# Optimization experiments

Measured on AMD Instinct MI355X. Metric: run time of the kernel, lower is better.

## Reference

```python
import jax, jax.numpy as jnp
import numpy as np

_K_MASK = float(jnp.finfo(jnp.float32).min)
EPS = 1e-6
B, T, D = 2, 2048, 2048
NH, NKV, HD = 16, 4, 128


def _rope_tables(key):
    # Standard RoPE tables: (B, T, HD) with [freqs, freqs] layout (rotate_half convention)
    inv_freq = 1.0 / (10000.0 ** (np.arange(0, HD, 2, dtype=np.float32) / HD))  # (HD/2,)
    pos = np.arange(T, dtype=np.float32)
    freqs = np.einsum('t,f->tf', pos, inv_freq)              # (T, HD/2)
    emb = np.concatenate([freqs, freqs], axis=-1)            # (T, HD)
    cos = jnp.broadcast_to(jnp.cos(emb)[None], (B, T, HD))
    sin = jnp.broadcast_to(jnp.sin(emb)[None], (B, T, HD))
    return cos, sin


def setup_inputs() -> dict:
    key = jax.random.key(0)
    ks = jax.random.split(key, 6)
    s = 0.02
    cos, sin = _rope_tables(key)
    return {
        'x': jax.random.normal(ks[0], (B, T, D), jnp.float32),
        'cos': cos,
        'sin': sin,
        'wq': jax.random.normal(ks[1], (D, NH * HD * 2), jnp.float32) * s,
        'wk': jax.random.normal(ks[2], (D, NKV * HD), jnp.float32) * s,
        'wv': jax.random.normal(ks[3], (D, NKV * HD), jnp.float32) * s,
        'wo': jax.random.normal(ks[4], (NH * HD, D), jnp.float32) * s,
        'q_norm_w': jnp.ones((HD,), jnp.float32),
        'k_norm_w': jnp.ones((HD,), jnp.float32),
        'segment_ids': jnp.ones((B, T), jnp.int32),
        'position_ids': jnp.broadcast_to(jnp.arange(T, dtype=jnp.int32)[None], (B, T)),
    }


def _rmsnorm(x, w):
    var = jnp.mean(jnp.square(x.astype(jnp.float32)), axis=-1, keepdims=True)
    return (x.astype(jnp.float32) * jax.lax.rsqrt(var + EPS)).astype(x.dtype) * w


def _rotate_half(x):
    x1, x2 = jnp.split(x, 2, axis=-1)
    return jnp.concatenate([-x2, x1], axis=-1)


def _apply_rope(q, k, cos, sin):
    # q: (B, NH, T, HD), k: (B, NKV, T, HD), cos/sin: (B, T, HD)
    c = cos[:, None, :, :]
    s = sin[:, None, :, :]
    q = q * c + _rotate_half(q) * s
    k = k * c + _rotate_half(k) * s
    return q, k


def reference(x, cos, sin, wq, wk, wv, wo, q_norm_w, k_norm_w, segment_ids, position_ids):
    Bx, Tx, _ = x.shape
    n_rep = NH // NKV
    scale = HD ** -0.5

    q_out = (x @ wq).reshape(Bx, Tx, NH, HD * 2)
    query, gate = jnp.split(q_out, 2, axis=-1)         # each (B, T, NH, HD)
    gate = gate.reshape(Bx, Tx, -1)                    # (B, T, NH*HD)
    query = _rmsnorm(query, q_norm_w).transpose(0, 2, 1, 3)   # (B, NH, T, HD)
    key = _rmsnorm((x @ wk).reshape(Bx, Tx, NKV, HD), k_norm_w).transpose(0, 2, 1, 3)
    value = (x @ wv).reshape(Bx, Tx, NKV, HD).transpose(0, 2, 1, 3)

    query, key = _apply_rope(query, key, cos, sin)
    if n_rep > 1:
        key = jnp.repeat(key, n_rep, axis=1)
        value = jnp.repeat(value, n_rep, axis=1)

    attn_logits = jnp.einsum('bhqd,bhkd->bhqk', query, key) * scale
    causal = position_ids[:, :, None] >= position_ids[:, None, :]
    seg = segment_ids[:, :, None] == segment_ids[:, None, :]
    mask = (causal & seg)[:, None, :, :]
    attn_logits = jnp.where(mask, attn_logits, _K_MASK)
    attn_weights = jax.nn.softmax(attn_logits.astype(jnp.float32), axis=-1).astype(attn_logits.dtype)
    attn_out = jnp.einsum('bhqk,bhkd->bhqd', attn_weights, value)
    attn_out = attn_out.transpose(0, 2, 1, 3).reshape(Bx, Tx, -1)  # (B, T, NH*HD)
    attn_out = attn_out * jax.nn.sigmoid(gate)
    return attn_out @ wo
```

## Files before the change

kernel.cpp:

```cpp
#include <hip/hip_runtime.h>

#define AS1 __attribute__((address_space(1)))
#define AS3 __attribute__((address_space(3)))

typedef __bf16 bf16x8 __attribute__((ext_vector_type(8)));
typedef float f32x4 __attribute__((ext_vector_type(4)));
typedef float f32x16 __attribute__((ext_vector_type(16)));
typedef unsigned short us8 __attribute__((ext_vector_type(8)));
typedef unsigned int u32x4 __attribute__((ext_vector_type(4)));

static constexpr int T_ = 2048;
static constexpr int NH_ = 16;
static constexpr int NKV_ = 4;
static constexpr int HD_ = 128;
static constexpr int NQKV_ = 5120;
static constexpr float SL2E_ = 0.12751744f;

static __device__ __forceinline__ unsigned short f2b(float f) {
  unsigned u = __builtin_bit_cast(unsigned, f);
  u += 0x7fffu + ((u >> 16) & 1u);
  return (unsigned short)(u >> 16);
}
static __device__ __forceinline__ float b2f(unsigned short h) {
  unsigned u = ((unsigned)h) << 16;
  return __builtin_bit_cast(float, u);
}
static __device__ __forceinline__ void load_lds16(const void* g, void* l) {
  __builtin_amdgcn_global_load_lds((const AS1 unsigned int*)g, (AS3 unsigned int*)l, 16, 0, 0);
}
static __device__ __forceinline__ f32x4 mfma16(bf16x8 a, bf16x8 b, f32x4 c) {
  return __builtin_amdgcn_mfma_f32_16x16x32_bf16(a, b, c, 0, 0, 0);
}
static __device__ __forceinline__ f32x16 mfma32(bf16x8 a, bf16x8 b, f32x16 c) {
  return __builtin_amdgcn_mfma_f32_32x32x16_bf16(a, b, c, 0, 0, 0);
}
static __device__ __forceinline__ unsigned cvtpk(float lo, float hi) {
  unsigned r;
  asm("v_cvt_pk_bf16_f32 %0, %1, %2" : "=v"(r) : "v"(lo), "v"(hi));
  return r;
}
static __device__ __forceinline__ void pl32swap(unsigned& a, unsigned& b) {
  asm("v_permlane32_swap_b32 %0, %1" : "+v"(a), "+v"(b));
}
#define S_BARRIER() asm volatile("s_barrier" ::: "memory")
#define VMCNT(n) asm volatile("s_waitcnt vmcnt(" #n ")" ::: "memory")

__global__ __launch_bounds__(256) void conv_bf16_kernel(
    const float* __restrict__ src, unsigned short* __restrict__ dst, int n) {
  int i = (blockIdx.x * 256 + threadIdx.x) * 4;
  if (i >= n) return;
  float4 v = *(const float4*)(src + i);
  ushort4 o;
  o.x = f2b(v.x); o.y = f2b(v.y); o.z = f2b(v.z); o.w = f2b(v.w);
  *(ushort4*)(dst + i) = o;
}

__global__ void tconv_kernel(const float* __restrict__ src, unsigned short* __restrict__ dst,
                             int R, int C, int roff) {
  __shared__ float tile[32][33];
  const int c0 = blockIdx.x * 32, r0 = blockIdx.y * 32;
#pragma unroll
  for (int j = 0; j < 32; j += 8)
    tile[threadIdx.y + j][threadIdx.x] =
        src[(size_t)(r0 + threadIdx.y + j) * C + c0 + threadIdx.x];
  __syncthreads();
#pragma unroll
  for (int j = 0; j < 32; j += 8)
    dst[(size_t)(roff + c0 + threadIdx.y + j) * R + r0 + threadIdx.x] =
        f2b(tile[threadIdx.x][threadIdx.y + j]);
}

template <int BF16OUT>
__global__ __launch_bounds__(512, 2) void gemm_bt8_kernel(
    const unsigned short* __restrict__ A, const unsigned short* __restrict__ Bt,
    void* __restrict__ Cv, unsigned short* __restrict__ Vt, int K, int N) {
  __shared__ __align__(16) unsigned short As[3][128 * 64];
  __shared__ __align__(16) unsigned short Bs[3][256 * 64];
  const int tid = threadIdx.x;
  const int wid = tid >> 6, lane = tid & 63;
  const int lq = lane & 15, lg = lane >> 4;
  const int l8 = lane >> 3, s8 = lane & 7;
  const int wr = wid >> 2, wc = wid & 3;
  const int brow = blockIdx.y * 128, bcol = blockIdx.x * 256;

  f32x4 acc[4][4];
#pragma unroll
  for (int m = 0; m < 4; ++m)
#pragma unroll
    for (int n = 0; n < 4; ++n) acc[m][n] = (f32x4){0.f, 0.f, 0.f, 0.f};

  auto STAGE_HALF = [&](int t, int b3t, int half) {
    const int k0 = t * 64;
    {
      const int ca = wid + half * 8;
      const int row = ca * 8 + l8;
      load_lds16(A + (size_t)(brow + row) * K + k0 + ((s8 ^ (row & 7)) << 3),
                 &As[b3t][ca << 9]);
    }
#pragma unroll
    for (int j = 0; j < 2; ++j) {
      const int cb = wid + half * 16 + (j << 3);
      const int row = cb * 8 + l8;
      load_lds16(Bt + (size_t)(bcol + row) * K + k0 + ((s8 ^ (row & 7)) << 3),
                 &Bs[b3t][cb << 9]);
    }
  };
  auto PHASE_READS = [&](int b3, int ks, bf16x8* a, bf16x8* bb) {
#pragma unroll
    for (int m = 0; m < 4; ++m) {
      const int r = wr * 64 + m * 16 + lq;
      a[m] = *(const bf16x8*)&As[b3][r * 64 + (((ks * 4 + lg) ^ (r & 7)) << 3)];
    }
#pragma unroll
    for (int n = 0; n < 4; ++n) {
      const int r = wc * 64 + n * 16 + lq;
      bb[n] = *(const bf16x8*)&Bs[b3][r * 64 + (((ks * 4 + lg) ^ (r & 7)) << 3)];
    }
  };
  auto DO_MFMA = [&](bf16x8* a, bf16x8* bb) {
    __builtin_amdgcn_s_setprio(1);
#pragma unroll
    for (int m = 0; m < 4; ++m)
#pragma unroll
      for (int n = 0; n < 4; ++n) acc[m][n] = mfma16(a[m], bb[n], acc[m][n]);
    __builtin_amdgcn_s_setprio(0);
  };

  STAGE_HALF(0, 0, 0); STAGE_HALF(0, 0, 1);
  STAGE_HALF(1, 1, 0); STAGE_HALF(1, 1, 1);
  VMCNT(6);
  S_BARRIER();

  int b3 = 0;
  for (int t = 0; t < 32; ++t) {
    const int b3p2 = b3 < 1 ? b3 + 2 : b3 - 1;
    bf16x8 a[4], bb[4];
    PHASE_READS(b3, 0, a, bb);
    if (t < 30) STAGE_HALF(t + 2, b3p2, 0);
    S_BARRIER();
    __builtin_amdgcn_sched_barrier(0);
    DO_MFMA(a, bb);
    S_BARRIER();
    PHASE_READS(b3, 1, a, bb);
    if (t < 30) STAGE_HALF(t + 2, b3p2, 1);
    if (t < 30) {
      VMCNT(6);
    } else if (t == 30) {
      VMCNT(0);
    }
    S_BARRIER();
    __builtin_amdgcn_sched_barrier(0);
    DO_MFMA(a, bb);
    if (t < 31) S_BARRIER();
    b3 = b3 < 2 ? b3 + 1 : 0;
  }
  if constexpr (BF16OUT) {
    if (bcol >= 4608) {
#pragma unroll
      for (int m = 0; m < 4; ++m) {
        const int R0 = brow + wr * 64 + m * 16 + lg * 4;
        const int bb2 = R0 >> 11, tt0 = R0 & 2047;
#pragma unroll
        for (int n = 0; n < 4; ++n) {
          const int vcol = bcol + wc * 64 + n * 16 + lq - 4608;
          const int vh = vcol >> 7, d = vcol & 127;
          ushort4 v4;
          v4.x = f2b(acc[m][n][0]); v4.y = f2b(acc[m][n][1]);
          v4.z = f2b(acc[m][n][2]); v4.w = f2b(acc[m][n][3]);
          *(ushort4*)&Vt[(size_t)((bb2 * 4 + vh) * 128 + d) * 2048 + tt0] = v4;
        }
      }
      return;
    }
  }
#pragma unroll
  for (int m = 0; m < 4; ++m)
#pragma unroll
    for (int n = 0; n < 4; ++n)
#pragma unroll
      for (int r = 0; r < 4; ++r) {
        const size_t idx =
            (size_t)(brow + wr * 64 + m * 16 + lg * 4 + r) * N + bcol + wc * 64 + n * 16 + lq;
        if constexpr (BF16OUT) {
          ((unsigned short*)Cv)[idx] = f2b(acc[m][n][r]);
        } else {
          ((float*)Cv)[idx] = acc[m][n][r];
        }
      }
}

__global__ __launch_bounds__(256) void postk_kernel(
    const unsigned short* __restrict__ qkv, const float* __restrict__ cosT,
    const float* __restrict__ sinT, const float* __restrict__ knw,
    unsigned short* __restrict__ Kg) {
  const int row = blockIdx.x * 4 + (threadIdx.x >> 6);
  const int b = row >> 11, t = row & 2047;
  const int lane = threadIdx.x & 63;
  const int kh = lane >> 4, sub = lane & 15;
  const int i0 = sub * 8;
  const bool lo = sub < 8;
  const unsigned short* src = qkv + (size_t)row * NQKV_ + 4096;

  us8 kv8 = *(const us8*)(src + kh * 128 + i0);
  float k[8], ss = 0.f;
#pragma unroll
  for (int j = 0; j < 8; ++j) { k[j] = b2f(kv8[j]); ss += k[j] * k[j]; }
  ss += __shfl_xor(ss, 1); ss += __shfl_xor(ss, 2);
  ss += __shfl_xor(ss, 4); ss += __shfl_xor(ss, 8);
  const float rms = rsqrtf(ss * (1.f / 128.f) + 1e-6f);
  float kn[8];
#pragma unroll
  for (int j = 0; j < 8; ++j) kn[j] = k[j] * rms * knw[i0 + j];
  float pr[8];
#pragma unroll
  for (int j = 0; j < 8; ++j) pr[j] = __shfl_xor(kn[j], 8);
  us8 ov;
#pragma unroll
  for (int j = 0; j < 8; ++j) {
    const float cs = cosT[(size_t)row * HD_ + i0 + j];
    const float sn = sinT[(size_t)row * HD_ + i0 + j];
    ov[j] = f2b(kn[j] * cs + (lo ? -pr[j] : pr[j]) * sn);
  }
  *(us8*)(Kg + ((size_t)(b * NKV_ + kh) * T_ + t) * HD_ + i0) = ov;
}

__global__ __launch_bounds__(256, 2) void attn_kernel(
    const unsigned short* __restrict__ Kg, const unsigned short* __restrict__ Vt,
    const unsigned short* __restrict__ qkv, const float* __restrict__ cosT,
    const float* __restrict__ sinT, const float* __restrict__ qnw,
    unsigned short* __restrict__ attnb) {
  __shared__ __align__(16) char smem[65536];
  const int i = blockIdx.x;
  const int xi = (i >> 3) & 15;
  const int grp = (i & 7) + ((i >> 7) << 3);
  const int h = grp & 15, b = grp >> 4;
  const int qt = b ? (15 - xi) : xi;
  const int kh = h >> 2;
  const int tid = threadIdx.x, wid = tid >> 6, lane = tid & 63;
  const int lq = lane & 31, hi = lane >> 5;
  const int q0 = qt * 128;
  const int qbase = q0 + wid * 32;
  const int qrow = qbase + lq;

  const char* Kbase = (const char*)(Kg + (size_t)(b * NKV_ + kh) * T_ * HD_);
  const char* Vbase = (const char*)(Vt + (size_t)(b * NKV_ + kh) * HD_ * T_);

  auto STAGE = [&](int tt, int c) {
    const int t0 = tt * 64;
    char* kd = smem + c * 32768;
    char* vd = kd + 16384;
#pragma unroll
    for (int j = 0; j < 4; ++j) {
      const int ch = j * 4 + wid;
      const int kv = ch * 4 + (lane >> 4);
      load_lds16(Kbase + (size_t)(t0 + kv) * 256 + (((lane & 15) ^ (kv & 7)) << 4),
                 kd + ch * 1024);
      const int dv = ch * 8 + (lane >> 3);
      load_lds16(Vbase + (size_t)dv * (T_ * 2) + (size_t)t0 * 2 +
                     (((lane & 7) ^ (dv & 7)) << 4),
                 vd + ch * 1024);
    }
  };

  STAGE(0, 0);

  const unsigned short* qraw = qkv + (size_t)(b * T_ + qrow) * NQKV_ + h * 256;
  float qv[8][8];
  float ss = 0.f;
#pragma unroll
  for (int t = 0; t < 8; ++t) {
    us8 v = *(const us8*)(qraw + t * 16 + hi * 8);
#pragma unroll
    for (int j = 0; j < 8; ++j) { qv[t][j] = b2f(v[j]); ss += qv[t][j] * qv[t][j]; }
  }
  ss += __shfl_xor(ss, 32);
  const float rms = rsqrtf(ss * (1.f / 128.f) + 1e-6f);
  const float* cosrow = cosT + (size_t)(b * T_ + qrow) * HD_;
  const float* sinrow = sinT + (size_t)(b * T_ + qrow) * HD_;
  bf16x8 qf[8];
#pragma unroll
  for (int t = 0; t < 8; ++t) {
    const int d0 = t * 16 + hi * 8;
    const int tp = (t < 4) ? t + 4 : t - 4;
    const int dp0 = tp * 16 + hi * 8;
    const float sgn = (t < 4) ? -1.f : 1.f;
    float ov[8];
#pragma unroll
    for (int j = 0; j < 8; ++j) {
      const float qn = qv[t][j] * rms * qnw[d0 + j];
      const float rot = sgn * qv[tp][j] * rms * qnw[dp0 + j];
      ov[j] = qn * cosrow[d0 + j] + rot * sinrow[d0 + j];
    }
    u32x4 w = {cvtpk(ov[0], ov[1]), cvtpk(ov[2], ov[3]),
               cvtpk(ov[4], ov[5]), cvtpk(ov[6], ov[7])};
    qf[t] = __builtin_bit_cast(bf16x8, w);
  }

  f32x16 o[4];
#pragma unroll
  for (int d = 0; d < 4; ++d)
#pragma unroll
    for (int r = 0; r < 16; ++r) o[d][r] = 0.f;
  float m_r = -1e30f, l_r = 0.f;
  const int nt = 2 * qt + 2;

  __syncthreads();
  int cur = 0;
  for (int tt = 0; tt < nt; ++tt) {
    const int t0 = tt * 64;
    if (tt + 1 < nt) STAGE(tt + 1, cur ^ 1);
    if (t0 <= qbase + 31) {
      const char* kd = smem + cur * 32768;
      const char* vd = kd + 16384;
      f32x16 sA, sB;
#pragma unroll
      for (int r = 0; r < 16; ++r) { sA[r] = 0.f; sB[r] = 0.f; }
      __builtin_amdgcn_s_setprio(1);
#pragma unroll
      for (int t = 0; t < 8; ++t) {
        const int sw = t * 2 + hi;
        bf16x8 ka = *(const bf16x8*)(kd + lq * 256 + ((sw ^ (lq & 7)) << 4));
        bf16x8 kb = *(const bf16x8*)(kd + (lq + 32) * 256 + ((sw ^ (lq & 7)) << 4));
        sA = mfma32(ka, qf[t], sA);
        sB = mfma32(kb, qf[t], sB);
      }
      __builtin_amdgcn_s_setprio(0);
      float p[32];
      float mx = -1e30f;
      const bool anymask = (t0 + 63 > qbase);
#pragma unroll
      for (int r = 0; r < 16; ++r) {
        const int kv = (r & 3) + ((r >> 2) << 3) + hi * 4;
        float vA = sA[r] * SL2E_;
        float vB = sB[r] * SL2E_;
        if (anymask) {
          if (t0 + kv > qrow) vA = -1e30f;
          if (t0 + kv + 32 > qrow) vB = -1e30f;
        }
        p[r] = vA; p[16 + r] = vB;
        mx = fmaxf(mx, fmaxf(vA, vB));
      }
      mx = fmaxf(mx, __shfl_xor(mx, 32));
      if (!__all(mx <= m_r + 8.f)) {
        const float mn = fmaxf(m_r, mx);
        const float al = exp2f(m_r - mn);
        l_r *= al;
#pragma unroll
        for (int d = 0; d < 4; ++d)
#pragma unroll
          for (int r = 0; r < 16; ++r) o[d][r] *= al;
        m_r = mn;
      }
      float sum = 0.f;
#pragma unroll
      for (int j = 0; j < 32; ++j) { p[j] = exp2f(p[j] - m_r); sum += p[j]; }
      sum += __shfl_xor(sum, 32);
      l_r += sum;
      bf16x8 pf[4];
#pragma unroll
      for (int kt = 0; kt < 4; ++kt) {
        const float* pp = p + kt * 8;
        unsigned a0 = cvtpk(pp[0], pp[1]);
        unsigned a1 = cvtpk(pp[2], pp[3]);
        unsigned b0 = cvtpk(pp[4], pp[5]);
        unsigned b1 = cvtpk(pp[6], pp[7]);
        pl32swap(a0, b0);
        pl32swap(a1, b1);
        u32x4 w = {a0, a1, b0, b1};
        pf[kt] = __builtin_bit_cast(bf16x8, w);
      }
      __builtin_amdgcn_s_setprio(1);
#pragma unroll
      for (int dt = 0; dt < 4; ++dt) {
        const int d = dt * 32 + lq;
#pragma unroll
        for (int kt = 0; kt < 4; ++kt) {
          bf16x8 vf = *(const bf16x8*)(vd + d * 128 + (((kt * 2 + hi) ^ (d & 7)) << 4));
          o[dt] = mfma32(vf, pf[kt], o[dt]);
        }
      }
      __builtin_amdgcn_s_setprio(0);
    }
    __syncthreads();
    cur ^= 1;
  }
  const float inv = 1.f / l_r;
  const unsigned short* grow = qkv + (size_t)(b * T_ + qrow) * NQKV_ + h * 256 + 128;
  unsigned short* orow = attnb + (size_t)(b * T_ + qrow) * (NH_ * HD_) + h * HD_;
#pragma unroll
  for (int dt = 0; dt < 4; ++dt)
#pragma unroll
    for (int g = 0; g < 4; ++g) {
      const int d0 = dt * 32 + g * 8 + hi * 4;
      ushort4 gv = *(const ushort4*)(grow + d0);
      ushort4 ov;
      ov.x = f2b(o[dt][g * 4 + 0] * inv / (1.f + __expf(-b2f(gv.x))));
      ov.y = f2b(o[dt][g * 4 + 1] * inv / (1.f + __expf(-b2f(gv.y))));
      ov.z = f2b(o[dt][g * 4 + 2] * inv / (1.f + __expf(-b2f(gv.z))));
      ov.w = f2b(o[dt][g * 4 + 3] * inv / (1.f + __expf(-b2f(gv.w))));
      *(ushort4*)(orow + d0) = ov;
    }
}

extern "C" void kernel_launch(void* const* d_in, const int* in_sizes, int n_in,
                              void* d_out, int out_size, void* d_ws, size_t ws_size,
                              hipStream_t stream) {
  (void)in_sizes; (void)n_in; (void)out_size; (void)ws_size;
  const float* x    = (const float*)d_in[0];
  const float* cosT = (const float*)d_in[1];
  const float* sinT = (const float*)d_in[2];
  const float* wq   = (const float*)d_in[3];
  const float* wk   = (const float*)d_in[4];
  const float* wv   = (const float*)d_in[5];
  const float* wo   = (const float*)d_in[6];
  const float* qnw  = (const float*)d_in[7];
  const float* knw  = (const float*)d_in[8];
  float* out = (float*)d_out;
  char* ws = (char*)d_ws;

  constexpr size_t OFF_XB    = 0;
  constexpr size_t OFF_WQKVT = OFF_XB    + (size_t)4096 * 2048 * 2;
  constexpr size_t OFF_WOT   = OFF_WQKVT + (size_t)5120 * 2048 * 2;
  constexpr size_t OFF_QKV   = OFF_WOT   + (size_t)2048 * 2048 * 2;
  constexpr size_t OFF_KG    = OFF_QKV   + (size_t)4096 * 5120 * 2;
  constexpr size_t OFF_VT    = OFF_KG    + (size_t)2 * 4 * 2048 * 128 * 2;
  constexpr size_t OFF_ATTNB = OFF_VT    + (size_t)2 * 4 * 128 * 2048 * 2;

  unsigned short* xb    = (unsigned short*)(ws + OFF_XB);
  unsigned short* wqkvT = (unsigned short*)(ws + OFF_WQKVT);
  unsigned short* woT   = (unsigned short*)(ws + OFF_WOT);
  unsigned short* qkv   = (unsigned short*)(ws + OFF_QKV);
  unsigned short* Kg    = (unsigned short*)(ws + OFF_KG);
  unsigned short* Vt    = (unsigned short*)(ws + OFF_VT);
  unsigned short* attnb = (unsigned short*)(ws + OFF_ATTNB);

  const int nX = 4096 * 2048;
  conv_bf16_kernel<<<nX / 4 / 256, 256, 0, stream>>>(x, xb, nX);
  tconv_kernel<<<dim3(4096 / 32, 2048 / 32), dim3(32, 8), 0, stream>>>(wq, wqkvT, 2048, 4096, 0);
  tconv_kernel<<<dim3(512 / 32, 2048 / 32), dim3(32, 8), 0, stream>>>(wk, wqkvT, 2048, 512, 4096);
  tconv_kernel<<<dim3(512 / 32, 2048 / 32), dim3(32, 8), 0, stream>>>(wv, wqkvT, 2048, 512, 4608);
  tconv_kernel<<<dim3(2048 / 32, 2048 / 32), dim3(32, 8), 0, stream>>>(wo, woT, 2048, 2048, 0);

  gemm_bt8_kernel<1><<<dim3(5120 / 256, 4096 / 128), 512, 0, stream>>>(
      xb, wqkvT, (void*)qkv, Vt, 2048, 5120);

  postk_kernel<<<1024, 256, 0, stream>>>(qkv, cosT, sinT, knw, Kg);

  attn_kernel<<<512, 256, 0, stream>>>(Kg, Vt, qkv, cosT, sinT, qnw, attnb);

  gemm_bt8_kernel<0><<<dim3(2048 / 256, 4096 / 128), 512, 0, stream>>>(
      attnb, woT, (void*)out, nullptr, 2048, 2048);
}
```

Measured before the change: 264.4 us.

## Shrink GEMM K-tile to 32 with single-phase triple-buffered pipeline

Changes the GEMM's K step from 64 to 32 per stage, halving the LDS buffers and switching the swizzle from 8-way to 4-way XOR. The main loop now runs one read/stage/MFMA phase per iteration over K/32 steps instead of two half-phases over 64-wide tiles, and the iteration count comes from K rather than a hardcoded 32. The smaller LDS footprint could allow more occupancy, but the loop needs twice as many barriers and waitcnt points per unit of work, and the 4-way swizzle may cause more bank conflicts.

After: 274.8 us. 1.04x slower.

```diff
diff --git a/kernel.cpp b/kernel.cpp
--- a/kernel.cpp
+++ b/kernel.cpp
@@ -74,14 +74,14 @@
 __global__ __launch_bounds__(512, 2) void gemm_bt8_kernel(
     const unsigned short* __restrict__ A, const unsigned short* __restrict__ Bt,
     void* __restrict__ Cv, unsigned short* __restrict__ Vt, int K, int N) {
-  __shared__ __align__(16) unsigned short As[3][128 * 64];
-  __shared__ __align__(16) unsigned short Bs[3][256 * 64];
+  __shared__ __align__(16) unsigned short As[3][128 * 32];
+  __shared__ __align__(16) unsigned short Bs[3][256 * 32];
   const int tid = threadIdx.x;
   const int wid = tid >> 6, lane = tid & 63;
   const int lq = lane & 15, lg = lane >> 4;
-  const int l8 = lane >> 3, s8 = lane & 7;
   const int wr = wid >> 2, wc = wid & 3;
   const int brow = blockIdx.y * 128, bcol = blockIdx.x * 256;
+  const int srow = lane >> 2, spc = lane & 3;
 
   f32x4 acc[4][4];
 #pragma unroll
@@ -89,70 +89,60 @@
 #pragma unroll
     for (int n = 0; n < 4; ++n) acc[m][n] = (f32x4){0.f, 0.f, 0.f, 0.f};
 
-  auto STAGE_HALF = [&](int t, int b3t, int half) {
-    const int k0 = t * 64;
+  auto STAGE = [&](int t, int q) {
+    const int k0 = t << 5;
     {
-      const int ca = wid + half * 8;
-      const int row = ca * 8 + l8;
-      load_lds16(A + (size_t)(brow + row) * K + k0 + ((s8 ^ (row & 7)) << 3),
-                 &As[b3t][ca << 9]);
+      const int row = wid * 16 + srow;
+      load_lds16(A + (size_t)(brow + row) * K + k0 + ((spc ^ (row & 3)) << 3),
+                 &As[q][wid << 9]);
     }
 #pragma unroll
     for (int j = 0; j < 2; ++j) {
-      const int cb = wid + half * 16 + (j << 3);
-      const int row = cb * 8 + l8;
-      load_lds16(Bt + (size_t)(bcol + row) * K + k0 + ((s8 ^ (row & 7)) << 3),
-                 &Bs[b3t][cb << 9]);
+      const int ch = wid * 2 + j;
+      const int row = ch * 16 + srow;
+      load_lds16(Bt + (size_t)(bcol + row) * K + k0 + ((spc ^ (row & 3)) << 3),
+                 &Bs[q][ch << 9]);
     }
   };
-  auto PHASE_READS = [&](int b3, int ks, bf16x8* a, bf16x8* bb) {
+  auto READS = [&](int q, bf16x8* a, bf16x8* bb) {
 #pragma unroll
     for (int m = 0; m < 4; ++m) {
       const int r = wr * 64 + m * 16 + lq;
-      a[m] = *(const bf16x8*)&As[b3][r * 64 + (((ks * 4 + lg) ^ (r & 7)) << 3)];
+      a[m] = *(const bf16x8*)&As[q][r * 32 + ((lg ^ (r & 3)) << 3)];
     }
 #pragma unroll
     for (int n = 0; n < 4; ++n) {
       const int r = wc * 64 + n * 16 + lq;
-      bb[n] = *(const bf16x8*)&Bs[b3][r * 64 + (((ks * 4 + lg) ^ (r & 7)) << 3)];
+      bb[n] = *(const bf16x8*)&Bs[q][r * 32 + ((lg ^ (r & 3)) << 3)];
     }
   };
-  auto DO_MFMA = [&](bf16x8* a, bf16x8* bb) {
+
+  STAGE(0, 0); STAGE(1, 1);
+  VMCNT(3);
+  S_BARRIER();
+
+  const int NT = K >> 5;
+  int q = 0;
+  for (int t = 0; t < NT; ++t) {
+    const int qp2 = q < 1 ? q + 2 : q - 1;
+    bf16x8 a[4], bb[4];
+    READS(q, a, bb);
+    if (t < NT - 2) {
+      STAGE(t + 2, qp2);
+      VMCNT(3);
+    } else if (t == NT - 2) {
+      VMCNT(0);
+    }
+    S_BARRIER();
+    __builtin_amdgcn_sched_barrier(0);
     __builtin_amdgcn_s_setprio(1);
 #pragma unroll
     for (int m = 0; m < 4; ++m)
 #pragma unroll
       for (int n = 0; n < 4; ++n) acc[m][n] = mfma16(a[m], bb[n], acc[m][n]);
     __builtin_amdgcn_s_setprio(0);
-  };
-
-  STAGE_HALF(0, 0, 0); STAGE_HALF(0, 0, 1);
-  STAGE_HALF(1, 1, 0); STAGE_HALF(1, 1, 1);
-  VMCNT(6);
-  S_BARRIER();
-
-  int b3 = 0;
-  for (int t = 0; t < 32; ++t) {
-    const int b3p2 = b3 < 1 ? b3 + 2 : b3 - 1;
-    bf16x8 a[4], bb[4];
-    PHASE_READS(b3, 0, a, bb);
-    if (t < 30) STAGE_HALF(t + 2, b3p2, 0);
-    S_BARRIER();
-    __builtin_amdgcn_sched_barrier(0);
-    DO_MFMA(a, bb);
-    S_BARRIER();
-    PHASE_READS(b3, 1, a, bb);
-    if (t < 30) STAGE_HALF(t + 2, b3p2, 1);
-    if (t < 30) {
-      VMCNT(6);
-    } else if (t == 30) {
-      VMCNT(0);
-    }
-    S_BARRIER();
-    __builtin_amdgcn_sched_barrier(0);
-    DO_MFMA(a, bb);
-    if (t < 31) S_BARRIER();
-    b3 = b3 < 2 ? b3 + 1 : 0;
+    if (t < NT - 1) S_BARRIER();
+    q = q < 2 ? q + 1 : 0;
   }
   if constexpr (BF16OUT) {
     if (bcol >= 4608) {
```
